# Kernel optimization log

Measured on AMD Instinct MI355X. Metric: run time of the kernel, lower is better.

Reference implementation:

```python
import jax, jax.numpy as jnp
import numpy as np

N_NODES = 50000
N_EDGES = 800000
NUM_FEAT = 100
F_DIM = 64
R_ROUNDS = 4
L_FP = 128
NUM_CLASS = 10


def setup_inputs() -> dict:
    key = jax.random.key(0)
    ks = jax.random.split(key, 10)
    s = 0.05
    return {
        "node_feature": jax.random.randint(ks[0], (N_NODES,), 0, NUM_FEAT),
        "edge_src": jax.random.randint(ks[1], (N_EDGES,), 0, N_NODES),
        "edge_dst": jax.random.randint(ks[2], (N_EDGES,), 0, N_NODES),
        "emb_table": jax.random.normal(ks[3], (NUM_FEAT, F_DIM), jnp.float32) * s,
        "W_h": jax.random.normal(ks[4], (R_ROUNDS, F_DIM, F_DIM), jnp.float32) * s,
        "b_h": jax.random.normal(ks[5], (R_ROUNDS, F_DIM), jnp.float32) * s,
        "W_fp": jax.random.normal(ks[6], (R_ROUNDS, F_DIM, L_FP), jnp.float32) * s,
        "b_fp": jax.random.normal(ks[7], (R_ROUNDS, L_FP), jnp.float32) * s,
        "W_cl": jax.random.normal(ks[8], (L_FP, NUM_CLASS), jnp.float32) * s,
        "b_cl": jax.random.normal(ks[9], (NUM_CLASS,), jnp.float32) * s,
    }


def reference(node_feature, edge_src, edge_dst, emb_table, W_h, b_h, W_fp, b_fp, W_cl, b_cl):
    # Initial node embeddings: [N, F]
    emb = emb_table[node_feature]
    f = jnp.zeros((L_FP,), dtype=emb.dtype)
    for r_i in range(R_ROUNDS):
        # v[node] = emb[node] + sum_{nbr in neighbours(node)} emb[nbr]
        agg = jax.ops.segment_sum(emb[edge_src], edge_dst, num_segments=N_NODES)
        v = emb + agg
        # per-node tiny MLP, batched over all nodes
        r = jax.nn.relu(v @ W_h[r_i] + b_h[r_i])            # [N, F]
        i = jax.nn.softmax(r @ W_fp[r_i] + b_fp[r_i], axis=-1)  # [N, L]
        f = f + i.sum(axis=0)                                # accumulate fingerprint
        emb = r                                              # synchronous update
    return jax.nn.softmax(f @ W_cl + b_cl, axis=-1)
```

## Files before the change

kernel.cpp:

```cpp
#include <hip/hip_runtime.h>
#include <hip/hip_bf16.h>

#define FDIM 64
#define LFP 128
#define RROUNDS 4
#define BM 64
#define PCHUNK 4096
#define CB 512
#define MAXB 10240
#define RSL 32

typedef __attribute__((ext_vector_type(8))) short bf16x8;
typedef __attribute__((ext_vector_type(4))) float f32x4;

__device__ __forceinline__ float bf2f(unsigned short u) {
    unsigned int x = ((unsigned int)u) << 16;
    float f;
    __builtin_memcpy(&f, &x, 4);
    return f;
}
__device__ __forceinline__ unsigned short f2bf(float x) {
    unsigned int u;
    __builtin_memcpy(&u, &x, 4);
    unsigned int r = (u + 0x7fffu + ((u >> 16) & 1u)) >> 16;
    return (unsigned short)r;
}

__global__ void setup_kernel(const int* __restrict__ feat, const float* __restrict__ table,
                             const float* __restrict__ Wh, const float* __restrict__ Wfp,
                             unsigned short* __restrict__ emb, unsigned short* __restrict__ whT,
                             unsigned short* __restrict__ wfpT, int* __restrict__ bucketCount,
                             int n) {
    int gid = blockIdx.x * blockDim.x + threadIdx.x;
    if (gid < RROUNDS * FDIM * FDIM) {
        int r = gid >> 12, rem = gid & 4095, j = rem >> 6, k = rem & 63;
        whT[gid] = f2bf(Wh[r * 4096 + k * 64 + j]);
    } else if (gid < RROUNDS * FDIM * FDIM + RROUNDS * LFP * FDIM) {
        int o2 = gid - RROUNDS * FDIM * FDIM;
        int r = o2 >> 13, rem = o2 & 8191, l = rem >> 6, k = rem & 63;
        wfpT[o2] = f2bf(Wfp[r * 8192 + k * 128 + l]);
    }
    if (gid < n * FDIM)
        emb[gid] = f2bf(table[feat[gid >> 6] * FDIM + (gid & 63)]);
    if (gid < 128) bucketCount[gid] = 0;
}

__global__ __launch_bounds__(256) void partition_kernel(
        const int* __restrict__ esrc, const int* __restrict__ edst,
        int* __restrict__ bucketCount, int* __restrict__ tmp, int nE, int nbc) {
    __shared__ int scnt[128], sinc[128], sexc[128], sgbase[128], scur[128];
    __shared__ int sbuf[PCHUNK];
    __shared__ int starg[PCHUNK];
    int t = threadIdx.x;
    int c0 = blockIdx.x * PCHUNK;
    int cend = c0 + PCHUNK; if (cend > nE) cend = nE;

    if (t < 128) scnt[t] = 0;
    __syncthreads();
#pragma unroll
    for (int k = 0; k < PCHUNK / 256; ++k) {
        int idx = c0 + k * 256 + t;
        if (idx < cend) atomicAdd(&scnt[edst[idx] >> 9], 1);
    }
    __syncthreads();
    if (t < 128) sinc[t] = scnt[t];
    __syncthreads();
    for (int d = 1; d < 128; d <<= 1) {
        int x = (t >= d && t < 128) ? sinc[t - d] : 0;
        __syncthreads();
        if (t < 128) sinc[t] += x;
        __syncthreads();
    }
    if (t < 128) {
        int ex = sinc[t] - scnt[t];
        sexc[t] = ex;
        scur[t] = ex;
        sgbase[t] = (t < nbc && scnt[t] > 0)
                        ? t * MAXB + atomicAdd(&bucketCount[t], scnt[t]) : 0;
    }
    __syncthreads();
#pragma unroll
    for (int k = 0; k < PCHUNK / 256; ++k) {
        int idx = c0 + k * 256 + t;
        if (idx < cend) {
            int s = esrc[idx], d = edst[idx];
            int b = d >> 9;
            int pos = atomicAdd(&scur[b], 1);
            sbuf[pos] = (s << 9) | (d & 511);
            starg[pos] = sgbase[b] + (pos - sexc[b]);
        }
    }
    __syncthreads();
    int cnt = cend - c0;
#pragma unroll
    for (int k = 0; k < PCHUNK / 256; ++k) {
        int li = k * 256 + t;
        if (li < cnt) tmp[starg[li]] = sbuf[li];
    }
}

__global__ __launch_bounds__(256) void bsort_kernel(
        const int* __restrict__ bucketCount, const int* __restrict__ tmp,
        unsigned short* __restrict__ csr16, int* __restrict__ rp, int N, int nE, int nbc) {
    __shared__ unsigned short ssrc[MAXB];
    __shared__ int pcnt[CB], pexc[CB], pcur[CB];
    __shared__ int ssum[256];
    __shared__ int sS[128];
    int t = threadIdx.x;
    int b = blockIdx.x;

    if (t < 128) sS[t] = (t < nbc) ? bucketCount[t] : 0;
    __syncthreads();
    for (int d = 1; d < 128; d <<= 1) {
        int x = (t >= d && t < 128) ? sS[t - d] : 0;
        __syncthreads();
        if (t < 128) sS[t] += x;
        __syncthreads();
    }
    int lo = (b == 0) ? 0 : sS[b - 1];
    int cnt = sS[b] - lo;

    pcnt[t] = 0; pcnt[t + 256] = 0;
    __syncthreads();
    const int* bt = tmp + (size_t)b * MAXB;
    for (int idx = t; idx < cnt; idx += 256)
        atomicAdd(&pcnt[bt[idx] & 511], 1);
    __syncthreads();
    int a0 = pcnt[2 * t], a1 = pcnt[2 * t + 1];
    ssum[t] = a0 + a1;
    __syncthreads();
    for (int d = 1; d < 256; d <<= 1) {
        int x = (t >= d) ? ssum[t - d] : 0;
        __syncthreads();
        ssum[t] += x;
        __syncthreads();
    }
    int ex = ssum[t] - (a0 + a1);
    pexc[2 * t] = ex;          pcur[2 * t] = ex;
    pexc[2 * t + 1] = ex + a0; pcur[2 * t + 1] = ex + a0;
    __syncthreads();
#pragma unroll
    for (int i = t; i < CB; i += 256) {
        int node = b * CB + i;
        if (node < N) rp[node] = lo + pexc[i];
    }
    if (b == 0 && t == 0) rp[N] = nE;
    for (int idx = t; idx < cnt; idx += 256) {
        int e = bt[idx];
        int pos = atomicAdd(&pcur[e & 511], 1);
        ssrc[pos] = (unsigned short)(e >> 9);
    }
    __syncthreads();
    for (int li = t; li < cnt; li += 256) csr16[lo + li] = ssrc[li];
}

__global__ __launch_bounds__(256) void gather_kernel(
        const unsigned short* __restrict__ emb, const int* __restrict__ rp,
        const unsigned short* __restrict__ csr16, unsigned short* __restrict__ vbuf, int N) {
    int wid = (int)((blockIdx.x * 256 + threadIdx.x) >> 6);
    int lane = threadIdx.x & 63;
    if (wid >= N) return;
    int start = rp[wid], end = rp[wid + 1];
    int last = end - 1;
    int grp = lane >> 3, q = lane & 7;

    bf16x8 self = *reinterpret_cast<const bf16x8*>(emb + (size_t)wid * 64 + q * 8);

    float acc[8] = {0.f, 0.f, 0.f, 0.f, 0.f, 0.f, 0.f, 0.f};
    for (int j = start + grp; j < end; j += 32) {
        int j1 = j + 8, j2 = j + 16, j3 = j + 24;
        int c1 = j1 <= last ? j1 : last;
        int c2 = j2 <= last ? j2 : last;
        int c3 = j3 <= last ? j3 : last;
        int n0 = csr16[j];
        int n1 = csr16[c1];
        int n2 = csr16[c2];
        int n3 = csr16[c3];
        bf16x8 u0 = *reinterpret_cast<const bf16x8*>(emb + (size_t)n0 * 64 + q * 8);
        bf16x8 u1 = *reinterpret_cast<const bf16x8*>(emb + (size_t)n1 * 64 + q * 8);
        bf16x8 u2 = *reinterpret_cast<const bf16x8*>(emb + (size_t)n2 * 64 + q * 8);
        bf16x8 u3 = *reinterpret_cast<const bf16x8*>(emb + (size_t)n3 * 64 + q * 8);
        float m1 = (j1 <= last) ? 1.f : 0.f;
        float m2 = (j2 <= last) ? 1.f : 0.f;
        float m3 = (j3 <= last) ? 1.f : 0.f;
#pragma unroll
        for (int x = 0; x < 8; ++x) {
            acc[x] += bf2f((unsigned short)u0[x]);
            acc[x] = fmaf(m1, bf2f((unsigned short)u1[x]), acc[x]);
            acc[x] = fmaf(m2, bf2f((unsigned short)u2[x]), acc[x]);
            acc[x] = fmaf(m3, bf2f((unsigned short)u3[x]), acc[x]);
        }
    }
#pragma unroll
    for (int x = 0; x < 8; ++x) {
        acc[x] += __shfl_xor(acc[x], 8);
        acc[x] += __shfl_xor(acc[x], 16);
        acc[x] += __shfl_xor(acc[x], 32);
    }
    if (grp == 0) {
        bf16x8 o;
#pragma unroll
        for (int x = 0; x < 8; ++x) o[x] = (short)f2bf(acc[x] + bf2f((unsigned short)self[x]));
        *reinterpret_cast<bf16x8*>(vbuf + (size_t)wid * 64 + q * 8) = o;
    }
}

__global__ __launch_bounds__(256) void mlp_kernel(
        const unsigned short* __restrict__ vbuf, unsigned short* __restrict__ emb_out,
        const unsigned short* __restrict__ whT, const unsigned short* __restrict__ wfpT,
        const float* __restrict__ bh, const float* __restrict__ bfp,
        float* __restrict__ fpart, int N) {
    __shared__ unsigned short sR[BM * 72];
    __shared__ float sFp[4][128];

    int tid = threadIdx.x;
    int base = blockIdx.x * BM;
    int lane = tid & 63, w = tid >> 6;
    int m16 = lane & 15, g = lane >> 4;
    int arow = w * 16 + m16;

    const unsigned short* vrow = vbuf + (size_t)(base + arow) * 64;
    bf16x8 a0 = *reinterpret_cast<const bf16x8*>(vrow + g * 8);
    bf16x8 a1 = *reinterpret_cast<const bf16x8*>(vrow + 32 + g * 8);

    f32x4 acc[4];
#pragma unroll
    for (int c = 0; c < 4; ++c) {
        bf16x8 b0 = *reinterpret_cast<const bf16x8*>(whT + (c * 16 + m16) * 64 + g * 8);
        bf16x8 b1 = *reinterpret_cast<const bf16x8*>(whT + (c * 16 + m16) * 64 + 32 + g * 8);
        f32x4 z = {0.f, 0.f, 0.f, 0.f};
        z = __builtin_amdgcn_mfma_f32_16x16x32_bf16(a0, b0, z, 0, 0, 0);
        z = __builtin_amdgcn_mfma_f32_16x16x32_bf16(a1, b1, z, 0, 0, 0);
        acc[c] = z;
    }
#pragma unroll
    for (int c = 0; c < 4; ++c) {
        float bias = bh[c * 16 + m16];
#pragma unroll
        for (int reg = 0; reg < 4; ++reg) {
            float rv = fmaxf(acc[c][reg] + bias, 0.f);
            sR[(w * 16 + g * 4 + reg) * 72 + c * 16 + m16] = f2bf(rv);
        }
    }

    bf16x8 ra0 = *reinterpret_cast<const bf16x8*>(sR + arow * 72 + g * 8);
    bf16x8 ra1 = *reinterpret_cast<const bf16x8*>(sR + arow * 72 + 32 + g * 8);

#pragma unroll
    for (int it = 0; it < 2; ++it) {
        int lidx = w * 1024 + it * 512 + lane * 8;
        int row = lidx >> 6;
        if (base + row < N)
            *reinterpret_cast<bf16x8*>(emb_out + (size_t)base * 64 + lidx) =
                *reinterpret_cast<const bf16x8*>(sR + row * 72 + (lidx & 63));
    }

    f32x4 z[8];
#pragma unroll
    for (int t = 0; t < 8; ++t) {
        bf16x8 b0 = *reinterpret_cast<const bf16x8*>(wfpT + (t * 16 + m16) * 64 + g * 8);
        bf16x8 b1 = *reinterpret_cast<const bf16x8*>(wfpT + (t * 16 + m16) * 64 + 32 + g * 8);
        f32x4 zz = {0.f, 0.f, 0.f, 0.f};
        zz = __builtin_amdgcn_mfma_f32_16x16x32_bf16(ra0, b0, zz, 0, 0, 0);
        zz = __builtin_amdgcn_mfma_f32_16x16x32_bf16(ra1, b1, zz, 0, 0, 0);
        float bias = bfp[t * 16 + m16];
#pragma unroll
        for (int reg = 0; reg < 4; ++reg) zz[reg] += bias;
        z[t] = zz;
    }

#pragma unroll
    for (int reg = 0; reg < 4; ++reg) {
        float mx = -1e30f;
#pragma unroll
        for (int t = 0; t < 8; ++t) mx = fmaxf(mx, z[t][reg]);
#pragma unroll
        for (int d = 1; d < 16; d <<= 1) mx = fmaxf(mx, __shfl_xor(mx, d));
        float s = 0.f;
#pragma unroll
        for (int t = 0; t < 8; ++t) {
            float p = __expf(z[t][reg] - mx);
            z[t][reg] = p;
            s += p;
        }
#pragma unroll
        for (int d = 1; d < 16; d <<= 1) s += __shfl_xor(s, d);
        int node = base + w * 16 + g * 4 + reg;
        float inv = (node < N) ? (1.f / s) : 0.f;
#pragma unroll
        for (int t = 0; t < 8; ++t) z[t][reg] *= inv;
    }
#pragma unroll
    for (int t = 0; t < 8; ++t) {
        float v = z[t][0] + z[t][1] + z[t][2] + z[t][3];
        v += __shfl_xor(v, 16);
        v += __shfl_xor(v, 32);
        if (g == 0) sFp[w][t * 16 + m16] = v;
    }
    __syncthreads();
    if (tid < 128) {
        float s = sFp[0][tid] + sFp[1][tid] + sFp[2][tid] + sFp[3][tid];
        fpart[(size_t)blockIdx.x * 128 + tid] = s;
    }
}

__global__ __launch_bounds__(256) void reduce1_kernel(const float* __restrict__ fpart,
                                                      float* __restrict__ fred, int nslice) {
    __shared__ float sAcc[128];
    int t = threadIdx.x;
    int col = t & 127, gp = t >> 7;
    int base = blockIdx.x * RSL + gp * (RSL / 2);
    const float* p = fpart + (size_t)base * 128 + col;
    float a0 = 0.f, a1 = 0.f, a2 = 0.f, a3 = 0.f;
    if (base + RSL / 2 <= nslice) {
#pragma unroll
        for (int k = 0; k < 4; ++k) {
            a0 += p[(k * 4 + 0) * 128];
            a1 += p[(k * 4 + 1) * 128];
            a2 += p[(k * 4 + 2) * 128];
            a3 += p[(k * 4 + 3) * 128];
        }
    } else {
        int cnt = nslice - base; if (cnt < 0) cnt = 0;
        for (int k = 0; k < cnt; ++k) a0 += p[k * 128];
    }
    float s = (a0 + a1) + (a2 + a3);
    if (gp == 1) sAcc[col] = s;
    __syncthreads();
    if (gp == 0) fred[(size_t)blockIdx.x * 128 + col] = s + sAcc[col];
}

__global__ __launch_bounds__(256) void final_kernel(const float* __restrict__ fred, int nred,
                                                    const float* __restrict__ Wcl,
                                                    const float* __restrict__ bcl,
                                                    float* __restrict__ out) {
    __shared__ float sAcc[128];
    __shared__ float sf[128];
    __shared__ float logits[10];
    int t = threadIdx.x;
    int col = t & 127, gp = t >> 7;
    int half = (nred + 1) >> 1;
    int b0 = gp * half;
    int b1 = b0 + half; if (b1 > nred) b1 = nred;
    float a0 = 0.f, a1 = 0.f, a2 = 0.f, a3 = 0.f;
    const float* p = fred + col;
    int b = b0;
    for (; b + 4 <= b1; b += 4) {
        a0 += p[(size_t)(b + 0) * 128];
        a1 += p[(size_t)(b + 1) * 128];
        a2 += p[(size_t)(b + 2) * 128];
        a3 += p[(size_t)(b + 3) * 128];
    }
    for (; b < b1; ++b) a0 += p[(size_t)b * 128];
    float s = (a0 + a1) + (a2 + a3);
    if (gp == 1) sAcc[col] = s;
    __syncthreads();
    if (gp == 0) sf[col] = s + sAcc[col];
    __syncthreads();
    if (t < 10) {
        float acc = bcl[t];
        for (int l = 0; l < LFP; l++) acc = fmaf(sf[l], Wcl[l * 10 + t], acc);
        logits[t] = acc;
    }
    __syncthreads();
    if (t == 0) {
        float m = -1e30f;
        for (int i = 0; i < 10; i++) m = fmaxf(m, logits[i]);
        float e[10], s2 = 0.f;
        for (int i = 0; i < 10; i++) { e[i] = __expf(logits[i] - m); s2 += e[i]; }
        for (int i = 0; i < 10; i++) out[i] = e[i] / s2;
    }
}

extern "C" void kernel_launch(void* const* d_in, const int* in_sizes, int n_in,
                              void* d_out, int out_size, void* d_ws, size_t ws_size,
                              hipStream_t stream) {
    const int* feat = (const int*)d_in[0];
    const int* esrc = (const int*)d_in[1];
    const int* edst = (const int*)d_in[2];
    const float* table = (const float*)d_in[3];
    const float* Wh = (const float*)d_in[4];
    const float* bh = (const float*)d_in[5];
    const float* Wfp = (const float*)d_in[6];
    const float* bfp = (const float*)d_in[7];
    const float* Wcl = (const float*)d_in[8];
    const float* bcl = (const float*)d_in[9];
    float* out = (float*)d_out;
    int N = in_sizes[0];
    int nE = in_sizes[1];

    int nbm = (N + BM - 1) / BM;
    int nbc = (N + CB - 1) / CB;
    int nbp = (nE + PCHUNK - 1) / PCHUNK;
    int nslice = RROUNDS * nbm;
    int nred = (nslice + RSL - 1) / RSL;

    char* ws = (char*)d_ws;
    size_t off = 0;
    auto alloc = [&](size_t bytes) { void* p = ws + off; off += (bytes + 63) & ~(size_t)63; return p; };
    unsigned short* embA = (unsigned short*)alloc((size_t)N * 64 * 2);
    unsigned short* vbuf = (unsigned short*)alloc((size_t)(N + BM) * 64 * 2);
    unsigned short* whT  = (unsigned short*)alloc(RROUNDS * 64 * 64 * 2);
    unsigned short* wfpT = (unsigned short*)alloc(RROUNDS * 128 * 64 * 2);
    float* fpart = (float*)alloc((size_t)nslice * 128 * 4);
    float* fred  = (float*)alloc((size_t)nred * 128 * 4);
    int* bucketCount = (int*)alloc(128 * 4);
    int* rp      = (int*)alloc(((size_t)N + 1) * 4);
    int* tmp     = (int*)alloc((size_t)nbc * MAXB * 4);
    unsigned short* csr16 = (unsigned short*)alloc((size_t)nE * 2);

    setup_kernel<<<(N * FDIM + 255) / 256, 256, 0, stream>>>(
        feat, table, Wh, Wfp, embA, whT, wfpT, bucketCount, N);

    partition_kernel<<<nbp, 256, 0, stream>>>(esrc, edst, bucketCount, tmp, nE, nbc);
    bsort_kernel<<<nbc, 256, 0, stream>>>(bucketCount, tmp, csr16, rp, N, nE, nbc);

    for (int r = 0; r < RROUNDS; ++r) {
        gather_kernel<<<(N * 64 + 255) / 256, 256, 0, stream>>>(embA, rp, csr16, vbuf, N);
        mlp_kernel<<<nbm, 256, 0, stream>>>(
            vbuf, embA, whT + (size_t)r * 4096, wfpT + (size_t)r * 8192,
            bh + (size_t)r * FDIM, bfp + (size_t)r * LFP,
            fpart + (size_t)r * nbm * 128, N);
    }

    reduce1_kernel<<<nred, 256, 0, stream>>>(fpart, fred, nslice);
    final_kernel<<<1, 256, 0, stream>>>(fred, nred, Wcl, bcl, out);
}
```

Baseline: 212.1 us.

## Fuse neighbor gather into MLP kernel with ping-pong embedding buffers

Merges the per-round gather and MLP kernels into one round_kernel. Each wave now aggregates 16 nodes one after another into shared memory, and the MFMA MLP reads them from there. This removes the vbuf round-trip through global memory and one launch per round. Embeddings alternate between two buffers to avoid read/write hazards. The cost is that the 782 blocks with serialized per-wave node loops have less parallelism and less latency hiding than the old one-wave-per-node gather, which had 12500 blocks.

```diff
diff --git a/kernel.cpp b/kernel.cpp
--- a/kernel.cpp
+++ b/kernel.cpp
@@ -154,74 +154,83 @@
     for (int li = t; li < cnt; li += 256) csr16[lo + li] = ssrc[li];
 }
 
-__global__ __launch_bounds__(256) void gather_kernel(
-        const unsigned short* __restrict__ emb, const int* __restrict__ rp,
-        const unsigned short* __restrict__ csr16, unsigned short* __restrict__ vbuf, int N) {
-    int wid = (int)((blockIdx.x * 256 + threadIdx.x) >> 6);
-    int lane = threadIdx.x & 63;
-    if (wid >= N) return;
-    int start = rp[wid], end = rp[wid + 1];
-    int last = end - 1;
-    int grp = lane >> 3, q = lane & 7;
-
-    bf16x8 self = *reinterpret_cast<const bf16x8*>(emb + (size_t)wid * 64 + q * 8);
-
-    float acc[8] = {0.f, 0.f, 0.f, 0.f, 0.f, 0.f, 0.f, 0.f};
-    for (int j = start + grp; j < end; j += 32) {
-        int j1 = j + 8, j2 = j + 16, j3 = j + 24;
-        int c1 = j1 <= last ? j1 : last;
-        int c2 = j2 <= last ? j2 : last;
-        int c3 = j3 <= last ? j3 : last;
-        int n0 = csr16[j];
-        int n1 = csr16[c1];
-        int n2 = csr16[c2];
-        int n3 = csr16[c3];
-        bf16x8 u0 = *reinterpret_cast<const bf16x8*>(emb + (size_t)n0 * 64 + q * 8);
-        bf16x8 u1 = *reinterpret_cast<const bf16x8*>(emb + (size_t)n1 * 64 + q * 8);
-        bf16x8 u2 = *reinterpret_cast<const bf16x8*>(emb + (size_t)n2 * 64 + q * 8);
-        bf16x8 u3 = *reinterpret_cast<const bf16x8*>(emb + (size_t)n3 * 64 + q * 8);
-        float m1 = (j1 <= last) ? 1.f : 0.f;
-        float m2 = (j2 <= last) ? 1.f : 0.f;
-        float m3 = (j3 <= last) ? 1.f : 0.f;
-#pragma unroll
-        for (int x = 0; x < 8; ++x) {
-            acc[x] += bf2f((unsigned short)u0[x]);
-            acc[x] = fmaf(m1, bf2f((unsigned short)u1[x]), acc[x]);
-            acc[x] = fmaf(m2, bf2f((unsigned short)u2[x]), acc[x]);
-            acc[x] = fmaf(m3, bf2f((unsigned short)u3[x]), acc[x]);
-        }
-    }
-#pragma unroll
-    for (int x = 0; x < 8; ++x) {
-        acc[x] += __shfl_xor(acc[x], 8);
-        acc[x] += __shfl_xor(acc[x], 16);
-        acc[x] += __shfl_xor(acc[x], 32);
-    }
-    if (grp == 0) {
-        bf16x8 o;
-#pragma unroll
-        for (int x = 0; x < 8; ++x) o[x] = (short)f2bf(acc[x] + bf2f((unsigned short)self[x]));
-        *reinterpret_cast<bf16x8*>(vbuf + (size_t)wid * 64 + q * 8) = o;
-    }
-}
-
-__global__ __launch_bounds__(256) void mlp_kernel(
-        const unsigned short* __restrict__ vbuf, unsigned short* __restrict__ emb_out,
+__global__ __launch_bounds__(256) void round_kernel(
+        const unsigned short* __restrict__ embIn, unsigned short* __restrict__ embOut,
+        const int* __restrict__ rp, const unsigned short* __restrict__ csr16,
         const unsigned short* __restrict__ whT, const unsigned short* __restrict__ wfpT,
         const float* __restrict__ bh, const float* __restrict__ bfp,
         float* __restrict__ fpart, int N) {
+    __shared__ unsigned short sV[BM * 72];
     __shared__ unsigned short sR[BM * 72];
     __shared__ float sFp[4][128];
 
     int tid = threadIdx.x;
     int base = blockIdx.x * BM;
     int lane = tid & 63, w = tid >> 6;
+    int grp = lane >> 3, q = lane & 7;
+
+    int nn = base + w * 16 + lane;
+    if (nn > N) nn = N;
+    int rpv = (lane < 17) ? rp[nn] : 0;
+
+#pragma unroll
+    for (int i = 0; i < 16; ++i) {
+        int node = base + w * 16 + i;
+        int start = __shfl(rpv, i);
+        int end = __shfl(rpv, i + 1);
+        if (node < N) {
+            int last = end - 1;
+            bf16x8 self = *reinterpret_cast<const bf16x8*>(embIn + (size_t)node * 64 + q * 8);
+            float acc[8] = {0.f, 0.f, 0.f, 0.f, 0.f, 0.f, 0.f, 0.f};
+            for (int j = start + grp; j < end; j += 32) {
+                int j1 = j + 8, j2 = j + 16, j3 = j + 24;
+                int c1 = j1 <= last ? j1 : last;
+                int c2 = j2 <= last ? j2 : last;
+                int c3 = j3 <= last ? j3 : last;
+                int n0 = csr16[j];
+                int n1 = csr16[c1];
+                int n2 = csr16[c2];
+                int n3 = csr16[c3];
+                bf16x8 u0 = *reinterpret_cast<const bf16x8*>(embIn + (size_t)n0 * 64 + q * 8);
+                bf16x8 u1 = *reinterpret_cast<const bf16x8*>(embIn + (size_t)n1 * 64 + q * 8);
+                bf16x8 u2 = *reinterpret_cast<const bf16x8*>(embIn + (size_t)n2 * 64 + q * 8);
+                bf16x8 u3 = *reinterpret_cast<const bf16x8*>(embIn + (size_t)n3 * 64 + q * 8);
+                float m1 = (j1 <= last) ? 1.f : 0.f;
+                float m2 = (j2 <= last) ? 1.f : 0.f;
+                float m3 = (j3 <= last) ? 1.f : 0.f;
+#pragma unroll
+                for (int x = 0; x < 8; ++x) {
+                    acc[x] += bf2f((unsigned short)u0[x]);
+                    acc[x] = fmaf(m1, bf2f((unsigned short)u1[x]), acc[x]);
+                    acc[x] = fmaf(m2, bf2f((unsigned short)u2[x]), acc[x]);
+                    acc[x] = fmaf(m3, bf2f((unsigned short)u3[x]), acc[x]);
+                }
+            }
+#pragma unroll
+            for (int x = 0; x < 8; ++x) {
+                acc[x] += __shfl_xor(acc[x], 8);
+                acc[x] += __shfl_xor(acc[x], 16);
+                acc[x] += __shfl_xor(acc[x], 32);
+            }
+            if (grp == 0) {
+                bf16x8 o;
+#pragma unroll
+                for (int x = 0; x < 8; ++x) o[x] = (short)f2bf(acc[x] + bf2f((unsigned short)self[x]));
+                *reinterpret_cast<bf16x8*>(sV + (w * 16 + i) * 72 + q * 8) = o;
+            }
+        } else if (grp == 0) {
+            bf16x8 o;
+#pragma unroll
+            for (int x = 0; x < 8; ++x) o[x] = 0;
+            *reinterpret_cast<bf16x8*>(sV + (w * 16 + i) * 72 + q * 8) = o;
+        }
+    }
+
     int m16 = lane & 15, g = lane >> 4;
     int arow = w * 16 + m16;
 
-    const unsigned short* vrow = vbuf + (size_t)(base + arow) * 64;
-    bf16x8 a0 = *reinterpret_cast<const bf16x8*>(vrow + g * 8);
-    bf16x8 a1 = *reinterpret_cast<const bf16x8*>(vrow + 32 + g * 8);
+    bf16x8 a0 = *reinterpret_cast<const bf16x8*>(sV + arow * 72 + g * 8);
+    bf16x8 a1 = *reinterpret_cast<const bf16x8*>(sV + arow * 72 + 32 + g * 8);
 
     f32x4 acc[4];
 #pragma unroll
@@ -251,7 +260,7 @@
         int lidx = w * 1024 + it * 512 + lane * 8;
         int row = lidx >> 6;
         if (base + row < N)
-            *reinterpret_cast<bf16x8*>(emb_out + (size_t)base * 64 + lidx) =
+            *reinterpret_cast<bf16x8*>(embOut + (size_t)base * 64 + lidx) =
                 *reinterpret_cast<const bf16x8*>(sR + row * 72 + (lidx & 63));
     }
 
@@ -399,7 +408,7 @@
     size_t off = 0;
     auto alloc = [&](size_t bytes) { void* p = ws + off; off += (bytes + 63) & ~(size_t)63; return p; };
     unsigned short* embA = (unsigned short*)alloc((size_t)N * 64 * 2);
-    unsigned short* vbuf = (unsigned short*)alloc((size_t)(N + BM) * 64 * 2);
+    unsigned short* embB = (unsigned short*)alloc((size_t)N * 64 * 2);
     unsigned short* whT  = (unsigned short*)alloc(RROUNDS * 64 * 64 * 2);
     unsigned short* wfpT = (unsigned short*)alloc(RROUNDS * 128 * 64 * 2);
     float* fpart = (float*)alloc((size_t)nslice * 128 * 4);
@@ -415,12 +424,14 @@
     partition_kernel<<<nbp, 256, 0, stream>>>(esrc, edst, bucketCount, tmp, nE, nbc);
     bsort_kernel<<<nbc, 256, 0, stream>>>(bucketCount, tmp, csr16, rp, N, nE, nbc);
 
+    unsigned short* eIn = embA;
+    unsigned short* eOut = embB;
     for (int r = 0; r < RROUNDS; ++r) {
-        gather_kernel<<<(N * 64 + 255) / 256, 256, 0, stream>>>(embA, rp, csr16, vbuf, N);
-        mlp_kernel<<<nbm, 256, 0, stream>>>(
-            vbuf, embA, whT + (size_t)r * 4096, wfpT + (size_t)r * 8192,
+        round_kernel<<<nbm, 256, 0, stream>>>(
+            eIn, eOut, rp, csr16, whT + (size_t)r * 4096, wfpT + (size_t)r * 8192,
             bh + (size_t)r * FDIM, bfp + (size_t)r * LFP,
             fpart + (size_t)r * nbm * 128, N);
+        unsigned short* t = eIn; eIn = eOut; eOut = t;
     }
 
     reduce1_kernel<<<nred, 256, 0, stream>>>(fpart, fred, nslice);
```

Result: no change. 210.1 us (-0.9%).
